# Kernel tuning notes

Measured on AMD Instinct MI355X. Metric: run time of the kernel, lower is better.

Reference implementation:

```python
import jax, jax.numpy as jnp
import numpy as np

B, T, D, H = 4, 2048, 1024, 16
HD = D // H  # 64
EPS = 1e-5

def _layernorm(x, g, b):
    mu = jnp.mean(x, axis=-1, keepdims=True)
    var = jnp.var(x, axis=-1, keepdims=True)
    return (x - mu) * jax.lax.rsqrt(var + EPS) * g + b

def setup_inputs() -> dict:
    key = jax.random.key(0)
    ks = jax.random.split(key, 8)
    s = D ** -0.5
    return {
        "x":  jax.random.normal(ks[0], (B, T, D), jnp.float32),
        "Wq": jax.random.normal(ks[1], (H, D, HD), jnp.float32) * s,
        "Wk": jax.random.normal(ks[2], (H, D, HD), jnp.float32) * s,
        "Wv": jax.random.normal(ks[3], (H, D, HD), jnp.float32) * s,
        "Wp": jax.random.normal(ks[4], (D, D), jnp.float32) * s,
        "bp": jnp.zeros((D,), jnp.float32),
        "W1": jax.random.normal(ks[5], (D, 4 * D), jnp.float32) * s,
        "b1": jnp.zeros((4 * D,), jnp.float32),
        "W2": jax.random.normal(ks[6], (4 * D, D), jnp.float32) * (4 * D) ** -0.5,
        "b2": jnp.zeros((D,), jnp.float32),
        "g1": jnp.ones((D,), jnp.float32),
        "be1": jnp.zeros((D,), jnp.float32),
        "g2": jnp.ones((D,), jnp.float32),
        "be2": jnp.zeros((D,), jnp.float32),
    }

def reference(x, Wq, Wk, Wv, Wp, bp, W1, b1, W2, b2, g1, be1, g2, be2):
    # --- pre-LN causal MHA (all heads batched; torch code loops per head) ---
    h = _layernorm(x, g1, be1)                       # [B,T,D]
    q = jnp.einsum('btd,hdk->bhtk', h, Wq)
    k = jnp.einsum('btd,hdk->bhtk', h, Wk)
    v = jnp.einsum('btd,hdk->bhtk', h, Wv)
    scores = jnp.einsum('bhtk,bhsk->bhts', q, k) * (HD ** -0.5)
    causal = jnp.tril(jnp.ones((T, T), bool))
    scores = jnp.where(causal, scores, -jnp.inf)
    w = jax.nn.softmax(scores, axis=-1)              # [B,H,T,T]
    o = jnp.einsum('bhts,bhsk->bhtk', w, v)          # [B,H,T,HD]
    o = o.transpose(0, 2, 1, 3).reshape(x.shape[0], x.shape[1], D)  # concat heads
    x = x + o @ Wp + bp                              # residual 1
    # --- pre-LN FFN ---
    h2 = _layernorm(x, g2, be2)
    ff = jax.nn.relu(h2 @ W1 + b1) @ W2 + b2
    return x + ff
```

## Files before the change

### kernel.cpp

```cpp
#include <hip/hip_runtime.h>
#include <hip/hip_bf16.h>
#include <math.h>

#define Bsz 4
#define Tsz 2048
#define Dsz 1024
#define Hn  16
#define HDs 64

typedef __attribute__((ext_vector_type(8))) short bf16x8;
typedef __attribute__((ext_vector_type(4))) float f32x4;

typedef const __attribute__((address_space(1))) void gvoid;
typedef __attribute__((address_space(3))) void lvoid;

__device__ __forceinline__ void async_copy16(const short* g, short* l) {
    __builtin_amdgcn_global_load_lds((gvoid*)g, (lvoid*)l, 16, 0, 0);
}

__device__ __forceinline__ short f2bf(float x) {
    __hip_bfloat16 h = __float2bfloat16(x);
    return *reinterpret_cast<short*>(&h);
}

__device__ __forceinline__ unsigned int pack_bf16(float hi, float lo) {
    unsigned int uh = __float_as_uint(hi) + 0x8000u;
    unsigned int ul = __float_as_uint(lo) + 0x8000u;
    return __builtin_amdgcn_perm(uh, ul, 0x07060302u);
}

__device__ __forceinline__ size_t headed_idx(int m, int c) {
    int b = m >> 11, t = m & 2047, h = c >> 6, kc = c & 63;
    return (((size_t)(b * Hn + h) * Tsz + t) << 6) + kc;
}

__global__ __launch_bounds__(256) void ln_kernel(const float* __restrict__ x,
                                                 const float* __restrict__ g,
                                                 const float* __restrict__ beta,
                                                 short* __restrict__ out)
{
    const int row = blockIdx.x;
    const float* xr = x + (size_t)row * Dsz;
    float v[4];
    float s = 0.f, s2 = 0.f;
#pragma unroll
    for (int i = 0; i < 4; ++i) {
        v[i] = xr[threadIdx.x + 256 * i];
        s += v[i];
        s2 += v[i] * v[i];
    }
#pragma unroll
    for (int off = 32; off; off >>= 1) {
        s  += __shfl_xor(s,  off);
        s2 += __shfl_xor(s2, off);
    }
    __shared__ float red[8];
    const int wave = threadIdx.x >> 6;
    if ((threadIdx.x & 63) == 0) { red[wave * 2] = s; red[wave * 2 + 1] = s2; }
    __syncthreads();
    s  = red[0] + red[2] + red[4] + red[6];
    s2 = red[1] + red[3] + red[5] + red[7];
    const float mu  = s * (1.f / Dsz);
    const float var = s2 * (1.f / Dsz) - mu * mu;
    const float rs  = rsqrtf(var + 1e-5f);
    short* orow = out + (size_t)row * Dsz;
#pragma unroll
    for (int i = 0; i < 4; ++i) {
        int col = threadIdx.x + 256 * i;
        orow[col] = f2bf((v[i] - mu) * rs * g[col] + beta[col]);
    }
}

__global__ __launch_bounds__(256) void transpose_cvt(
    const float* __restrict__ in, short* __restrict__ outp, int R, int C)
{
    __shared__ float tile[32][33];
    const int r0 = blockIdx.y * 32, c0 = blockIdx.x * 32;
    const size_t so = (size_t)blockIdx.z * R * C;
    const int tx = threadIdx.x & 31, ty = threadIdx.x >> 5;
    const float* ip = in + so;
    short* op = outp + so;
#pragma unroll
    for (int i = 0; i < 4; ++i)
        tile[ty + i * 8][tx] = ip[(size_t)(r0 + ty + i * 8) * C + c0 + tx];
    __syncthreads();
#pragma unroll
    for (int i = 0; i < 4; ++i)
        op[(size_t)(c0 + ty + i * 8) * R + r0 + tx] = f2bf(tile[tx][ty + i * 8]);
}

__global__ __launch_bounds__(256) void transpose_cvt_qkv(
    const float* __restrict__ Wq, const float* __restrict__ Wk,
    const float* __restrict__ Wv, short* __restrict__ outp)
{
    __shared__ float tile[32][33];
    const int z = blockIdx.z;
    const float* in = (z < 16) ? Wq : (z < 32) ? Wk : Wv;
    const int zz = z & 15;
    const int r0 = blockIdx.y * 32, c0 = blockIdx.x * 32;
    const int tx = threadIdx.x & 31, ty = threadIdx.x >> 5;
    const float* ip = in + (size_t)zz * (1024 * 64);
    short* op = outp + (size_t)z * (1024 * 64);
#pragma unroll
    for (int i = 0; i < 4; ++i)
        tile[ty + i * 8][tx] = ip[(size_t)(r0 + ty + i * 8) * 64 + c0 + tx];
    __syncthreads();
#pragma unroll
    for (int i = 0; i < 4; ++i)
        op[(size_t)(c0 + ty + i * 8) * 1024 + r0 + tx] = f2bf(tile[tx][ty + i * 8]);
}

template <int EPI>
__global__ __launch_bounds__(256) void gemm_mfma(
    const short* __restrict__ A, const short* __restrict__ Bt,
    const float* __restrict__ bias, const float* __restrict__ resid,
    float* __restrict__ Cf, short* __restrict__ Cb0,
    short* __restrict__ Cb1, short* __restrict__ Cb2,
    int M, int N, int K, float scale)
{
    __shared__ short As[128 * 32];
    __shared__ short Bs[128 * 32];
    const int tid  = threadIdx.x;
    const int lane = tid & 63, wave = tid >> 6;
    const int quad = lane >> 4, l16 = lane & 15;

    const int lin = blockIdx.y * gridDim.x + blockIdx.x;
    const int xcd = lin & 7;
    const int s   = lin >> 3;
    const int my  = xcd * 8 + (s & 7);
    const int nx  = s >> 3;
    const int m0 = my * 128, n0 = nx * 128;

    const int wm = (wave >> 1) * 64, wn = (wave & 1) * 64;

    f32x4 acc[4][4];
#pragma unroll
    for (int i = 0; i < 4; ++i)
#pragma unroll
        for (int j = 0; j < 4; ++j) acc[i][j] = f32x4{0.f, 0.f, 0.f, 0.f};

    const short* gA = A  + (size_t)(m0 + wave * 32 + (lane >> 2)) * K + (lane & 3) * 8;
    const short* gB = Bt + (size_t)(n0 + wave * 32 + (lane >> 2)) * K + (lane & 3) * 8;
    short* lA0 = As + wave * 1024;
    short* lA1 = As + wave * 1024 + 512;
    short* lB0 = Bs + wave * 1024;
    short* lB1 = Bs + wave * 1024 + 512;
    const size_t rstep = (size_t)16 * K;

    for (int k0 = 0; k0 < K; k0 += 32) {
        async_copy16(gA,         lA0);
        async_copy16(gA + rstep, lA1);
        async_copy16(gB,         lB0);
        async_copy16(gB + rstep, lB1);
        gA += 32; gB += 32;
        __syncthreads();
        bf16x8 af[4], bfr[4];
#pragma unroll
        for (int mt = 0; mt < 4; ++mt)
            af[mt] = *(const bf16x8*)(As + (wm + mt * 16 + l16) * 32 + quad * 8);
#pragma unroll
        for (int nt = 0; nt < 4; ++nt)
            bfr[nt] = *(const bf16x8*)(Bs + (wn + nt * 16 + l16) * 32 + quad * 8);
#pragma unroll
        for (int mt = 0; mt < 4; ++mt)
#pragma unroll
            for (int nt = 0; nt < 4; ++nt)
                acc[mt][nt] = __builtin_amdgcn_mfma_f32_16x16x32_bf16(
                    af[mt], bfr[nt], acc[mt][nt], 0, 0, 0);
        __syncthreads();
    }

#pragma unroll
    for (int mt = 0; mt < 4; ++mt) {
#pragma unroll
        for (int nt = 0; nt < 4; ++nt) {
#pragma unroll
            for (int r = 0; r < 4; ++r) {
                const int m = m0 + wm + mt * 16 + quad * 4 + r;
                const int c = n0 + wn + nt * 16 + l16;
                float val = acc[mt][nt][r];
                if (EPI == 0) {
                    const int sel = c >> 10, cl = c & 1023;
                    if (sel == 0)
                        Cb0[headed_idx(m, cl)] = f2bf(val * scale);
                    else if (sel == 1)
                        Cb1[headed_idx(m, cl)] = f2bf(val);
                    else {
                        int b = m >> 11, t = m & 2047;
                        size_t idx = ((((size_t)((b << 4) | (cl >> 6)) << 6) | (cl & 63)) << 11) | t;
                        Cb2[idx] = f2bf(val);
                    }
                } else if (EPI == 2) {
                    size_t idx = (size_t)m * N + c;
                    Cf[idx] = val + bias[c] + resid[idx];
                } else {
                    float v2 = val + bias[c];
                    Cb0[(size_t)m * N + c] = f2bf(v2 > 0.f ? v2 : 0.f);
                }
            }
        }
    }
}

__global__ __launch_bounds__(256) void gemm_n64(
    const short* __restrict__ A, const short* __restrict__ Bt,
    const float* __restrict__ bias, const float* __restrict__ resid,
    float* __restrict__ Cf, int M, int N, int K)
{
    __shared__ short As[128 * 64];
    __shared__ short Bs[64 * 64];
    const int tid  = threadIdx.x;
    const int lane = tid & 63, wave = tid >> 6;
    const int quad = lane >> 4, l16 = lane & 15;

    const int lin = blockIdx.y * 16 + blockIdx.x;
    const int xcd = lin & 7;
    const int s   = lin >> 3;
    const int m0  = (xcd * 8 + (s & 7)) * 128;
    const int n0  = (s >> 3) * 64;

    const int wm = (wave >> 1) * 64, wn = (wave & 1) * 32;

    f32x4 acc[4][2];
#pragma unroll
    for (int i = 0; i < 4; ++i)
#pragma unroll
        for (int j = 0; j < 2; ++j) acc[i][j] = f32x4{0.f, 0.f, 0.f, 0.f};

    const short* gA[4];
    const short* gB[2];
    short* lA[4];
    short* lB[2];
#pragma unroll
    for (int i = 0; i < 4; ++i) {
        const int sl = tid + 256 * i, r = sl >> 3, g = (sl & 7) ^ (r & 7);
        gA[i] = A + (size_t)(m0 + r) * K + g * 8;
        lA[i] = As + sl * 8;
    }
#pragma unroll
    for (int i = 0; i < 2; ++i) {
        const int sl = tid + 256 * i, r = sl >> 3, g = (sl & 7) ^ (r & 7);
        gB[i] = Bt + (size_t)(n0 + r) * K + g * 8;
        lB[i] = Bs + sl * 8;
    }

    for (int k0 = 0; k0 < K; k0 += 64) {
#pragma unroll
        for (int i = 0; i < 4; ++i) { async_copy16(gA[i], lA[i]); gA[i] += 64; }
#pragma unroll
        for (int i = 0; i < 2; ++i) { async_copy16(gB[i], lB[i]); gB[i] += 64; }
        __syncthreads();
        bf16x8 af[4][2], bfr[2][2];
#pragma unroll
        for (int mt = 0; mt < 4; ++mt) {
            const int r = wm + mt * 16 + l16;
            af[mt][0] = *(const bf16x8*)(As + r * 64 + (((quad    ) ^ (r & 7)) << 3));
            af[mt][1] = *(const bf16x8*)(As + r * 64 + (((quad + 4) ^ (r & 7)) << 3));
        }
#pragma unroll
        for (int nt = 0; nt < 2; ++nt) {
            const int r = wn + nt * 16 + l16;
            bfr[nt][0] = *(const bf16x8*)(Bs + r * 64 + (((quad    ) ^ (r & 7)) << 3));
            bfr[nt][1] = *(const bf16x8*)(Bs + r * 64 + (((quad + 4) ^ (r & 7)) << 3));
        }
#pragma unroll
        for (int mt = 0; mt < 4; ++mt)
#pragma unroll
            for (int nt = 0; nt < 2; ++nt) {
                acc[mt][nt] = __builtin_amdgcn_mfma_f32_16x16x32_bf16(
                    af[mt][0], bfr[nt][0], acc[mt][nt], 0, 0, 0);
                acc[mt][nt] = __builtin_amdgcn_mfma_f32_16x16x32_bf16(
                    af[mt][1], bfr[nt][1], acc[mt][nt], 0, 0, 0);
            }
        __syncthreads();
    }

#pragma unroll
    for (int mt = 0; mt < 4; ++mt) {
#pragma unroll
        for (int nt = 0; nt < 2; ++nt) {
#pragma unroll
            for (int r = 0; r < 4; ++r) {
                const int m = m0 + wm + mt * 16 + quad * 4 + r;
                const int c = n0 + wn + nt * 16 + l16;
                const size_t idx = (size_t)m * N + c;
                Cf[idx] = acc[mt][nt][r] + bias[c] + resid[idx];
            }
        }
    }
}

__global__ __launch_bounds__(256, 4) void fattn_kernel(
    const short* __restrict__ Q,
    const short* __restrict__ K,
    const short* __restrict__ VT,
    short* __restrict__ O)
{
    __shared__ short Kl[2][64 * 64];
    __shared__ short Vl[2][64 * 64];
    __shared__ short p_lds[4][16 * 64];
    const int tid  = threadIdx.x;
    const int lane = tid & 63, wave = tid >> 6;
    const int quad = lane >> 4, l16 = lane & 15;

    const int lin  = blockIdx.y * 16 + blockIdx.x;
    const int xcd  = lin & 7;
    const int slot = lin >> 3;
    const int bh   = xcd * 8 + (slot >> 4);
    const int px   = slot & 15;
    const int tiles[2] = { 31 - px, px };

    const int bb = bh >> 4, hh = bh & 15;
    const size_t bhoff = (size_t)bh * (Tsz * HDs);
    const short* Qb = Q + bhoff;
    const short* Kb = K + bhoff;
    const short* Vb = VT + bhoff;

    const int s_a = tid, s_b = tid + 256;
    const int ra = s_a >> 3, ga = (s_a & 7) ^ (ra & 7);
    const int rb = s_b >> 3, gb = (s_b & 7) ^ (rb & 7);

    short* pw = &p_lds[wave][0];
    const int rd0 = l16 * 64 + (((quad    ) ^ (l16 & 7)) << 3);
    const int rd1 = l16 * 64 + (((quad + 4) ^ (l16 & 7)) << 3);

    bf16x8 bq[2][2];
#pragma unroll
    for (int ti = 0; ti < 2; ++ti) {
        const short* qp = Qb + (size_t)(tiles[ti] * 64 + wave * 16 + l16) * 64 + quad * 8;
        bq[ti][0] = *(const bf16x8*)qp;
        bq[ti][1] = *(const bf16x8*)(qp + 32);
    }

    auto stage = [&](int c64, int buf) {
        short* kb_l = &Kl[buf][0];
        short* vb_l = &Vl[buf][0];
        async_copy16(Kb + (((size_t)(c64 + ra)) << 6) + (ga << 3), kb_l + s_a * 8);
        async_copy16(Kb + (((size_t)(c64 + rb)) << 6) + (gb << 3), kb_l + s_b * 8);
        async_copy16(Vb + ((size_t)ra << 11) + c64 + (ga << 3), vb_l + s_a * 8);
        async_copy16(Vb + ((size_t)rb << 11) + c64 + (gb << 3), vb_l + s_b * 8);
    };

    stage(tiles[0] * 0, 0);
    __syncthreads();

    int phase = 0;
#pragma unroll
    for (int ti = 0; ti < 2; ++ti) {
        const int tile = tiles[ti];
        const int q0w  = tile * 64 + wave * 16;
        const int nch  = tile + 1;

        f32x4 oaccT[4];
        float lacc = 0.f;
#pragma unroll
        for (int nt = 0; nt < 4; ++nt) oaccT[nt] = f32x4{0.f, 0.f, 0.f, 0.f};

        for (int c = 0; c < nch; ++c) {
            const int cur = phase & 1;
            if (c + 1 < nch)   stage((c + 1) * 64, cur ^ 1);
            else if (ti == 0)  stage(0, cur ^ 1);

            const int s0 = c * 64;
            const short* Kc = &Kl[cur][0];
            const short* Vc = &Vl[cur][0];
            bf16x8 ak[4][2], av[4][2];
#pragma unroll
            for (int ct = 0; ct < 4; ++ct) {
                const int r = ct * 16 + l16;
                ak[ct][0] = *(const bf16x8*)(Kc + r * 64 + (((quad    ) ^ (r & 7)) << 3));
                ak[ct][1] = *(const bf16x8*)(Kc + r * 64 + (((quad + 4) ^ (r & 7)) << 3));
            }
#pragma unroll
            for (int nt = 0; nt < 4; ++nt) {
                const int r = nt * 16 + l16;
                av[nt][0] = *(const bf16x8*)(Vc + r * 64 + (((quad    ) ^ (r & 7)) << 3));
                av[nt][1] = *(const bf16x8*)(Vc + r * 64 + (((quad + 4) ^ (r & 7)) << 3));
            }
            f32x4 sfr[4];
#pragma unroll
            for (int ct = 0; ct < 4; ++ct) {
                f32x4 cc = {0.f, 0.f, 0.f, 0.f};
                cc = __builtin_amdgcn_mfma_f32_16x16x32_bf16(ak[ct][0], bq[ti][0], cc, 0, 0, 0);
                cc = __builtin_amdgcn_mfma_f32_16x16x32_bf16(ak[ct][1], bq[ti][1], cc, 0, 0, 0);
                sfr[ct] = cc;
            }
            if (s0 + 63 > q0w) {
                const int qr = q0w + l16;
#pragma unroll
                for (int ct = 0; ct < 4; ++ct)
#pragma unroll
                    for (int r = 0; r < 4; ++r)
                        if (s0 + ct * 16 + quad * 4 + r > qr)
                            sfr[ct][r] = -INFINITY;
            }
#pragma unroll
            for (int ct = 0; ct < 4; ++ct) {
                float p0 = __builtin_exp2f(sfr[ct][0]);
                float p1 = __builtin_exp2f(sfr[ct][1]);
                float p2 = __builtin_exp2f(sfr[ct][2]);
                float p3 = __builtin_exp2f(sfr[ct][3]);
                lacc += (p0 + p1) + (p2 + p3);
                uint2 pkv;
                pkv.x = pack_bf16(p1, p0);
                pkv.y = pack_bf16(p3, p2);
                const int g = (2 * ct + (quad >> 1)) ^ (l16 & 7);
                *(uint2*)(pw + l16 * 64 + (g << 3) + (quad & 1) * 4) = pkv;
            }
            bf16x8 bp0 = *(const bf16x8*)(pw + rd0);
            bf16x8 bp1 = *(const bf16x8*)(pw + rd1);
#pragma unroll
            for (int nt = 0; nt < 4; ++nt) {
                oaccT[nt] = __builtin_amdgcn_mfma_f32_16x16x32_bf16(av[nt][0], bp0, oaccT[nt], 0, 0, 0);
                oaccT[nt] = __builtin_amdgcn_mfma_f32_16x16x32_bf16(av[nt][1], bp1, oaccT[nt], 0, 0, 0);
            }
            __syncthreads();
            ++phase;
        }

        float ps = lacc;
        ps += __shfl_xor(ps, 16);
        ps += __shfl_xor(ps, 32);
        const float inv = 1.f / ps;
        short* orow = O + (size_t)(bb * Tsz + q0w + l16) * Dsz + hh * 64;
#pragma unroll
        for (int nt = 0; nt < 4; ++nt) {
            uint2 pkv;
            pkv.x = pack_bf16(oaccT[nt][1] * inv, oaccT[nt][0] * inv);
            pkv.y = pack_bf16(oaccT[nt][3] * inv, oaccT[nt][2] * inv);
            *(uint2*)(orow + nt * 16 + quad * 4) = pkv;
        }
    }
}

extern "C" void kernel_launch(void* const* d_in, const int* in_sizes, int n_in,
                              void* d_out, int out_size, void* d_ws, size_t ws_size,
                              hipStream_t stream) {
    const float* x   = (const float*)d_in[0];
    const float* Wq  = (const float*)d_in[1];
    const float* Wk  = (const float*)d_in[2];
    const float* Wv  = (const float*)d_in[3];
    const float* Wp  = (const float*)d_in[4];
    const float* bp  = (const float*)d_in[5];
    const float* W1  = (const float*)d_in[6];
    const float* b1  = (const float*)d_in[7];
    const float* W2  = (const float*)d_in[8];
    const float* b2  = (const float*)d_in[9];
    const float* g1  = (const float*)d_in[10];
    const float* be1 = (const float*)d_in[11];
    const float* g2  = (const float*)d_in[12];
    const float* be2 = (const float*)d_in[13];
    float* out = (float*)d_out;
    char*  W   = (char*)d_ws;

    short* h1  = (short*)(W);
    short* ff1 = (short*)(W);
    short* qb  = (short*)(W + (16ull << 20));
    short* kb  = (short*)(W + (32ull << 20));
    short* vtb = (short*)(W + (48ull << 20));
    short* o   = (short*)(W + (64ull << 20));
    short* h2  = (short*)(W + (80ull << 20));
    short* wqt = (short*)(W + (96ull << 20));
    short* wpt = (short*)(W + (102ull << 20));
    short* w1t = (short*)(W + (104ull << 20));
    short* w2t = (short*)(W + (112ull << 20));

    const int M = Bsz * Tsz;
    const float qscale = 0.125f * 1.44269504f;

    transpose_cvt_qkv<<<dim3(2, 32, 48), 256, 0, stream>>>(Wq, Wk, Wv, wqt);
    transpose_cvt<<<dim3(32, 32, 1),  256, 0, stream>>>(Wp, wpt, 1024, 1024);
    transpose_cvt<<<dim3(128, 32, 1), 256, 0, stream>>>(W1, w1t, 1024, 4096);
    transpose_cvt<<<dim3(32, 128, 1), 256, 0, stream>>>(W2, w2t, 4096, 1024);

    ln_kernel<<<dim3(M), 256, 0, stream>>>(x, g1, be1, h1);

    gemm_mfma<0><<<dim3(24, 64), 256, 0, stream>>>(
        h1, wqt, nullptr, nullptr, nullptr, qb, kb, vtb, M, 3072, 1024, qscale);

    fattn_kernel<<<dim3(16, Bsz * Hn), 256, 0, stream>>>(qb, kb, vtb, o);

    gemm_n64<<<dim3(16, 64), 256, 0, stream>>>(
        o, wpt, bp, x, out, M, 1024, 1024);

    ln_kernel<<<dim3(M), 256, 0, stream>>>(out, g2, be2, h2);

    gemm_mfma<3><<<dim3(32, 64), 256, 0, stream>>>(
        h2, w1t, b1, nullptr, nullptr, ff1, nullptr, nullptr, M, 4096, 1024, 1.f);

    gemm_n64<<<dim3(16, 64), 256, 0, stream>>>(
        ff1, w2t, b2, out, out, M, 1024, 4096);
}
```

Baseline: 553.1 us.

## Double-buffer LDS tiles in GEMM kernels to overlap global loads with MFMA

Both GEMM kernels now use two LDS buffers per operand. The next K-tile's global-to-LDS async copy is issued before the MFMA work on the current tile, and a prologue loads the first tile. This aims to hide global load latency behind compute. It doubles LDS usage, which can lower occupancy. It relies on the single barrier at the end of each iteration for correctness, and the async copies to the next buffer may not be waited on explicitly before that barrier.

```diff
diff --git a/kernel.cpp b/kernel.cpp
--- a/kernel.cpp
+++ b/kernel.cpp
@@ -118,8 +118,8 @@
     short* __restrict__ Cb1, short* __restrict__ Cb2,
     int M, int N, int K, float scale)
 {
-    __shared__ short As[128 * 32];
-    __shared__ short Bs[128 * 32];
+    __shared__ short As[2][128 * 32];
+    __shared__ short Bs[2][128 * 32];
     const int tid  = threadIdx.x;
     const int lane = tid & 63, wave = tid >> 6;
     const int quad = lane >> 4, l16 = lane & 15;
@@ -141,26 +141,33 @@
 
     const short* gA = A  + (size_t)(m0 + wave * 32 + (lane >> 2)) * K + (lane & 3) * 8;
     const short* gB = Bt + (size_t)(n0 + wave * 32 + (lane >> 2)) * K + (lane & 3) * 8;
-    short* lA0 = As + wave * 1024;
-    short* lA1 = As + wave * 1024 + 512;
-    short* lB0 = Bs + wave * 1024;
-    short* lB1 = Bs + wave * 1024 + 512;
     const size_t rstep = (size_t)16 * K;
-
+    const int woff = wave * 1024;
+
+    async_copy16(gA,         &As[0][woff]);
+    async_copy16(gA + rstep, &As[0][woff + 512]);
+    async_copy16(gB,         &Bs[0][woff]);
+    async_copy16(gB + rstep, &Bs[0][woff + 512]);
+    gA += 32; gB += 32;
+    __syncthreads();
+
+    int cur = 0;
     for (int k0 = 0; k0 < K; k0 += 32) {
-        async_copy16(gA,         lA0);
-        async_copy16(gA + rstep, lA1);
-        async_copy16(gB,         lB0);
-        async_copy16(gB + rstep, lB1);
-        gA += 32; gB += 32;
-        __syncthreads();
+        if (k0 + 32 < K) {
+            const int nxt = cur ^ 1;
+            async_copy16(gA,         &As[nxt][woff]);
+            async_copy16(gA + rstep, &As[nxt][woff + 512]);
+            async_copy16(gB,         &Bs[nxt][woff]);
+            async_copy16(gB + rstep, &Bs[nxt][woff + 512]);
+            gA += 32; gB += 32;
+        }
         bf16x8 af[4], bfr[4];
 #pragma unroll
         for (int mt = 0; mt < 4; ++mt)
-            af[mt] = *(const bf16x8*)(As + (wm + mt * 16 + l16) * 32 + quad * 8);
+            af[mt] = *(const bf16x8*)(&As[cur][(wm + mt * 16 + l16) * 32 + quad * 8]);
 #pragma unroll
         for (int nt = 0; nt < 4; ++nt)
-            bfr[nt] = *(const bf16x8*)(Bs + (wn + nt * 16 + l16) * 32 + quad * 8);
+            bfr[nt] = *(const bf16x8*)(&Bs[cur][(wn + nt * 16 + l16) * 32 + quad * 8]);
 #pragma unroll
         for (int mt = 0; mt < 4; ++mt)
 #pragma unroll
@@ -168,6 +175,7 @@
                 acc[mt][nt] = __builtin_amdgcn_mfma_f32_16x16x32_bf16(
                     af[mt], bfr[nt], acc[mt][nt], 0, 0, 0);
         __syncthreads();
+        cur ^= 1;
     }
 
 #pragma unroll
@@ -207,8 +215,8 @@
     const float* __restrict__ bias, const float* __restrict__ resid,
     float* __restrict__ Cf, int M, int N, int K)
 {
-    __shared__ short As[128 * 64];
-    __shared__ short Bs[64 * 64];
+    __shared__ short As[2][128 * 64];
+    __shared__ short Bs[2][64 * 64];
     const int tid  = threadIdx.x;
     const int lane = tid & 63, wave = tid >> 6;
     const int quad = lane >> 4, l16 = lane & 15;
@@ -229,39 +237,47 @@
 
     const short* gA[4];
     const short* gB[2];
-    short* lA[4];
-    short* lB[2];
+    int dA[4], dB[2];
 #pragma unroll
     for (int i = 0; i < 4; ++i) {
         const int sl = tid + 256 * i, r = sl >> 3, g = (sl & 7) ^ (r & 7);
         gA[i] = A + (size_t)(m0 + r) * K + g * 8;
-        lA[i] = As + sl * 8;
+        dA[i] = sl * 8;
     }
 #pragma unroll
     for (int i = 0; i < 2; ++i) {
         const int sl = tid + 256 * i, r = sl >> 3, g = (sl & 7) ^ (r & 7);
         gB[i] = Bt + (size_t)(n0 + r) * K + g * 8;
-        lB[i] = Bs + sl * 8;
-    }
-
+        dB[i] = sl * 8;
+    }
+
+#pragma unroll
+    for (int i = 0; i < 4; ++i) { async_copy16(gA[i], &As[0][dA[i]]); gA[i] += 64; }
+#pragma unroll
+    for (int i = 0; i < 2; ++i) { async_copy16(gB[i], &Bs[0][dB[i]]); gB[i] += 64; }
+    __syncthreads();
+
+    int cur = 0;
     for (int k0 = 0; k0 < K; k0 += 64) {
-#pragma unroll
-        for (int i = 0; i < 4; ++i) { async_copy16(gA[i], lA[i]); gA[i] += 64; }
-#pragma unroll
-        for (int i = 0; i < 2; ++i) { async_copy16(gB[i], lB[i]); gB[i] += 64; }
-        __syncthreads();
+        if (k0 + 64 < K) {
+            const int nxt = cur ^ 1;
+#pragma unroll
+            for (int i = 0; i < 4; ++i) { async_copy16(gA[i], &As[nxt][dA[i]]); gA[i] += 64; }
+#pragma unroll
+            for (int i = 0; i < 2; ++i) { async_copy16(gB[i], &Bs[nxt][dB[i]]); gB[i] += 64; }
+        }
         bf16x8 af[4][2], bfr[2][2];
 #pragma unroll
         for (int mt = 0; mt < 4; ++mt) {
             const int r = wm + mt * 16 + l16;
-            af[mt][0] = *(const bf16x8*)(As + r * 64 + (((quad    ) ^ (r & 7)) << 3));
-            af[mt][1] = *(const bf16x8*)(As + r * 64 + (((quad + 4) ^ (r & 7)) << 3));
+            af[mt][0] = *(const bf16x8*)(&As[cur][r * 64 + (((quad    ) ^ (r & 7)) << 3)]);
+            af[mt][1] = *(const bf16x8*)(&As[cur][r * 64 + (((quad + 4) ^ (r & 7)) << 3)]);
         }
 #pragma unroll
         for (int nt = 0; nt < 2; ++nt) {
             const int r = wn + nt * 16 + l16;
-            bfr[nt][0] = *(const bf16x8*)(Bs + r * 64 + (((quad    ) ^ (r & 7)) << 3));
-            bfr[nt][1] = *(const bf16x8*)(Bs + r * 64 + (((quad + 4) ^ (r & 7)) << 3));
+            bfr[nt][0] = *(const bf16x8*)(&Bs[cur][r * 64 + (((quad    ) ^ (r & 7)) << 3)]);
+            bfr[nt][1] = *(const bf16x8*)(&Bs[cur][r * 64 + (((quad + 4) ^ (r & 7)) << 3)]);
         }
 #pragma unroll
         for (int mt = 0; mt < 4; ++mt)
@@ -273,6 +289,7 @@
                     af[mt][1], bfr[nt][1], acc[mt][nt], 0, 0, 0);
             }
         __syncthreads();
+        cur ^= 1;
     }
 
 #pragma unroll
```

After: 537.9 us. -2.7%, faster.
